# Kernel optimization log

Measured on AMD Instinct MI355X. Metric: run time of the kernel, lower is better.

Reference implementation:

```python
import jax, jax.numpy as jnp
import numpy as np

D_MODEL = 768
D_STATE = 16
D_CONV = 4
EXPAND = 2
D_INNER = EXPAND * D_MODEL  # 1536
DT_RANK = -(-D_MODEL // 16)  # ceil(768/16) = 48
BATCH = 1
SEQ = 2048


def _silu(v):
    return v * jax.nn.sigmoid(v)


def setup_inputs() -> dict:
    key = jax.random.key(0)
    ks = jax.random.split(key, 8)
    s = 0.02
    x = jax.random.normal(ks[0], (BATCH, SEQ, D_MODEL), jnp.float32)
    in_proj_w = jax.random.normal(ks[1], (2 * D_INNER, D_MODEL), jnp.float32) * s
    conv_w = jax.random.normal(ks[2], (D_INNER, 1, D_CONV), jnp.float32) * s  # depthwise, groups=D_INNER
    conv_b = jnp.zeros((D_INNER,), jnp.float32)
    x_proj_w = jax.random.normal(ks[3], (DT_RANK + 2 * D_STATE, D_INNER), jnp.float32) * s
    dt_proj_w = jax.random.normal(ks[4], (D_INNER, DT_RANK), jnp.float32) * s
    dt_proj_b = jax.random.normal(ks[5], (D_INNER,), jnp.float32) * 0.01
    # A = repeat_interleave(arange(1, d_state+1), d_inner rows); A_log = log(A)
    A_log = jnp.log(jnp.tile(jnp.arange(1, D_STATE + 1, dtype=jnp.float32)[None, :], (D_INNER, 1)))
    D = jnp.ones((D_INNER,), jnp.float32)
    out_proj_w = jax.random.normal(ks[6], (D_MODEL, D_INNER), jnp.float32) * s
    return {"x": x, "in_proj_w": in_proj_w, "conv_w": conv_w, "conv_b": conv_b,
            "x_proj_w": x_proj_w, "dt_proj_w": dt_proj_w, "dt_proj_b": dt_proj_b,
            "A_log": A_log, "D": D, "out_proj_w": out_proj_w}


def reference(x, in_proj_w, conv_w, conv_b, x_proj_w, dt_proj_w, dt_proj_b, A_log, D, out_proj_w):
    b, L, d = x.shape
    # in_proj then split into x-branch and gate z
    xz = x @ in_proj_w.T                       # (b, L, 2*d_inner)
    xh, z = jnp.split(xz, 2, axis=-1)          # each (b, L, d_inner)
    # causal depthwise conv1d: torch pads d_conv-1 both sides then slices [:L];
    # equivalent to left-pad d_conv-1, right-pad 0
    xc = jnp.transpose(xh, (0, 2, 1))          # (b, d_inner, L)
    xc = jax.lax.conv_general_dilated(
        xc, conv_w, window_strides=(1,), padding=[(D_CONV - 1, 0)],
        feature_group_count=D_INNER, dimension_numbers=("NCH", "OIH", "NCH"))
    xc = xc + conv_b[None, :, None]
    u = _silu(jnp.transpose(xc, (0, 2, 1)))    # (b, L, d_inner)
    # input-dependent dt, B, C
    x_dbl = u @ x_proj_w.T                     # (b, L, dt_rank + 2*d_state)
    dt, Bm, Cm = jnp.split(x_dbl, [DT_RANK, DT_RANK + D_STATE], axis=-1)
    dt = jax.nn.softplus(dt @ dt_proj_w.T + dt_proj_b)  # (b, L, d_inner)
    A = -jnp.exp(A_log)                        # (d_inner, d_state)
    # selective scan via cumprod/cumsum (faithful to source math)
    dA = jnp.exp(dt[..., None] * A[None, None])              # (b, L, d_inner, d_state)
    dBu = dt[..., None] * Bm[:, :, None, :] * u[..., None]   # (b, L, d_inner, d_state)
    p = jnp.cumprod(dA, axis=1)
    eps = jnp.finfo(u.dtype).eps
    p_safe = jnp.maximum(p, eps)
    g = jnp.cumsum(dBu / p_safe, axis=1)
    h = g * p
    y = jnp.sum(h * Cm[:, :, None, :], axis=-1) + D * u      # (b, L, d_inner)
    y = y * _silu(z)
    return y @ out_proj_w.T                    # (b, L, d_model); dropout=identity (eval)
```

## Files before the change

kernel.cpp:

```cpp
#include <hip/hip_runtime.h>
#include <hip/hip_bf16.h>

#define LSEQ 2048
#define DMODEL 768
#define DINNER 1536
#define DSTATE 16
#define DTRANK 48
#define XDBL_W (DTRANK + 2*DSTATE)
#define CHUNK 32
#define NCHUNK (LSEQ / CHUNK)
#define NDN (DINNER * DSTATE)
#define FEPS 1.1920928955078125e-07f
#define SPLITK 8
#define OSPLIT 4
#define LDST2 36

typedef short bf16x8 __attribute__((ext_vector_type(8)));
typedef float f32x4 __attribute__((ext_vector_type(4)));
typedef unsigned short u16;

__device__ __forceinline__ u16 f2bf_rn(float f) {
    unsigned u = __float_as_uint(f);
    unsigned r = u + 0x7FFFu + ((u >> 16) & 1u);
    return (u16)(r >> 16);
}
__device__ __forceinline__ float bf2f(u16 h) {
    return __uint_as_float(((unsigned)h) << 16);
}

template<int CTRL>
__device__ __forceinline__ float qperm(float x) {
    return __int_as_float(__builtin_amdgcn_update_dpp(
        0, __float_as_int(x), CTRL, 0xF, 0xF, true));
}

__global__ __launch_bounds__(256) void cvt_split(
    const float* __restrict__ src, u16* __restrict__ hi, u16* __restrict__ lo, int n)
{
    int i = (blockIdx.x * 256 + threadIdx.x) * 4;
    if (i >= n) return;
    float4 v = *(const float4*)&src[i];
    u16 h0 = f2bf_rn(v.x), h1 = f2bf_rn(v.y), h2 = f2bf_rn(v.z), h3 = f2bf_rn(v.w);
    u16 l0 = f2bf_rn(v.x - bf2f(h0));
    u16 l1 = f2bf_rn(v.y - bf2f(h1));
    u16 l2 = f2bf_rn(v.z - bf2f(h2));
    u16 l3 = f2bf_rn(v.w - bf2f(h3));
    *(ushort4*)&hi[i] = make_ushort4(h0, h1, h2, h3);
    *(ushort4*)&lo[i] = make_ushort4(l0, l1, l2, l3);
}

__global__ __launch_bounds__(256) void mfma_gemm_tn(
    const u16* __restrict__ Ahi, const u16* __restrict__ Alo,
    const u16* __restrict__ Bhi, const u16* __restrict__ Blo,
    float* __restrict__ C, int ldc, int ldk, int Klen)
{
    __shared__ u16 lds[2 * 4 * 4096];
    const int tid = threadIdx.x;
    const int wid = tid >> 6;
    const int lane = tid & 63;
    const int m0 = blockIdx.x * 128;
    const int n0 = blockIdx.y * 128;
    const int Koff = blockIdx.z * Klen;

    const int st_subrow = lane >> 2;
    const int st_cphys = lane & 3;
    const u16* myplane = (wid == 0) ? Ahi : (wid == 1) ? Alo : (wid == 2) ? Bhi : Blo;
    const int rowbase = (wid < 2) ? m0 : n0;

    f32x4 acc[4][4] = {};
    const int wm = (wid >> 1) * 64;
    const int wn = (wid & 1) * 64;
    const int fr = lane & 15;
    const int fc = lane >> 4;
    const int nsteps = Klen / 32;

    auto stage = [&](int buf, int k0) {
#pragma unroll
        for (int j = 0; j < 8; ++j) {
            int row = j * 16 + st_subrow;
            int clog = st_cphys ^ ((row >> 1) & 3);
            const u16* g = myplane + (size_t)(rowbase + row) * ldk + k0 + clog * 8;
            u16* l = &lds[buf * 16384 + wid * 4096 + j * 512];
            __builtin_amdgcn_global_load_lds(
                (const __attribute__((address_space(1))) unsigned int*)g,
                (__attribute__((address_space(3))) unsigned int*)l, 16, 0, 0);
        }
    };

    stage(0, Koff);
    int cur = 0;
    for (int t = 0; t < nsteps; ++t) {
        __syncthreads();
        if (t + 1 < nsteps) stage(cur ^ 1, Koff + (t + 1) * 32);

        bf16x8 ah[4], al[4], bh[4], bl[4];
        const bf16x8* L = (const bf16x8*)&lds[cur * 16384];
#pragma unroll
        for (int mi = 0; mi < 4; ++mi) {
            int r = wm + mi * 16 + fr;
            int idx = r * 4 + (fc ^ ((r >> 1) & 3));
            ah[mi] = L[idx];
            al[mi] = L[512 + idx];
        }
#pragma unroll
        for (int nj = 0; nj < 4; ++nj) {
            int r = wn + nj * 16 + fr;
            int idx = r * 4 + (fc ^ ((r >> 1) & 3));
            bh[nj] = L[1024 + idx];
            bl[nj] = L[1536 + idx];
        }
#pragma unroll
        for (int mi = 0; mi < 4; ++mi)
#pragma unroll
            for (int nj = 0; nj < 4; ++nj) {
                acc[mi][nj] = __builtin_amdgcn_mfma_f32_16x16x32_bf16(ah[mi], bh[nj], acc[mi][nj], 0, 0, 0);
                acc[mi][nj] = __builtin_amdgcn_mfma_f32_16x16x32_bf16(ah[mi], bl[nj], acc[mi][nj], 0, 0, 0);
                acc[mi][nj] = __builtin_amdgcn_mfma_f32_16x16x32_bf16(al[mi], bh[nj], acc[mi][nj], 0, 0, 0);
            }
        cur ^= 1;
    }

    float* Cz = C + (size_t)blockIdx.z * LSEQ * ldc;
#pragma unroll
    for (int mi = 0; mi < 4; ++mi) {
        int row_b = m0 + wm + mi * 16 + (lane >> 4) * 4;
#pragma unroll
        for (int nj = 0; nj < 4; ++nj) {
            int col = n0 + wn + nj * 16 + (lane & 15);
#pragma unroll
            for (int r = 0; r < 4; ++r)
                Cz[(size_t)(row_b + r) * ldc + col] = acc[mi][nj][r];
        }
    }
}

__global__ __launch_bounds__(256) void reduce4(
    const float* __restrict__ Ppart, float* __restrict__ out, int n)
{
    int i = (blockIdx.x * 256 + threadIdx.x) * 4;
    if (i >= n) return;
    float4 a0 = *(const float4*)&Ppart[i];
    float4 a1 = *(const float4*)&Ppart[(size_t)n + i];
    float4 a2 = *(const float4*)&Ppart[(size_t)2 * n + i];
    float4 a3 = *(const float4*)&Ppart[(size_t)3 * n + i];
    float4 r;
    r.x = ((a0.x + a1.x) + a2.x) + a3.x;
    r.y = ((a0.y + a1.y) + a2.y) + a3.y;
    r.z = ((a0.z + a1.z) + a2.z) + a3.z;
    r.w = ((a0.w + a1.w) + a2.w) + a3.w;
    *(float4*)&out[i] = r;
}

template<int EPI>
__global__ __launch_bounds__(256) void gemm_tn(
    const float* __restrict__ A, int lda,
    const float* __restrict__ B, int ldb,
    float* __restrict__ C, int ldc,
    int M, int N, int K,
    const float* __restrict__ bias)
{
    __shared__ float As[16][64 + 4];
    __shared__ float Bs[16][64 + 4];
    const int tid = threadIdx.x;
    const int m0 = blockIdx.x * 64;
    const int n0 = blockIdx.y * 64;
    const int tx = tid & 15;
    const int ty = tid >> 4;
    const int lr = tid >> 4;
    const int lc = tid & 15;
    float acc[4][4] = {};

    for (int k0 = 0; k0 < K; k0 += 16) {
        const int k = k0 + lc;
#pragma unroll
        for (int i = 0; i < 4; ++i) {
            int m = m0 + lr + i * 16;
            As[lc][lr + i * 16] = (m < M) ? A[(size_t)m * lda + k] : 0.f;
        }
#pragma unroll
        for (int i = 0; i < 4; ++i) {
            int n = n0 + lr + i * 16;
            Bs[lc][lr + i * 16] = (n < N) ? B[(size_t)n * ldb + k] : 0.f;
        }
        __syncthreads();
#pragma unroll
        for (int kk = 0; kk < 16; ++kk) {
            float a[4], b[4];
#pragma unroll
            for (int i = 0; i < 4; ++i) a[i] = As[kk][ty * 4 + i];
#pragma unroll
            for (int j = 0; j < 4; ++j) b[j] = Bs[kk][tx * 4 + j];
#pragma unroll
            for (int i = 0; i < 4; ++i)
#pragma unroll
                for (int j = 0; j < 4; ++j)
                    acc[i][j] = fmaf(a[i], b[j], acc[i][j]);
        }
        __syncthreads();
    }

#pragma unroll
    for (int i = 0; i < 4; ++i) {
        int m = m0 + ty * 4 + i;
        if (m >= M) continue;
#pragma unroll
        for (int j = 0; j < 4; ++j) {
            int n = n0 + tx * 4 + j;
            if (n >= N) continue;
            float v = acc[i][j];
            if (EPI == 1) {
                v += bias[n];
                v = fmaxf(v, 0.f) + log1pf(expf(-fabsf(v)));
            }
            C[(size_t)m * ldc + n] = v;
        }
    }
}

__global__ __launch_bounds__(256) void gemm_tn_splitk(
    const float* __restrict__ A, int lda,
    const float* __restrict__ B, int ldb,
    float* __restrict__ Cpart, int ldc,
    int M, int N, int Kchunk)
{
    __shared__ float As[16][64 + 4];
    __shared__ float Bs[16][64 + 4];
    const int tid = threadIdx.x;
    const int m0 = blockIdx.x * 64;
    const int n0 = blockIdx.y * 64;
    const int kb = blockIdx.z * Kchunk;
    const int tx = tid & 15;
    const int ty = tid >> 4;
    const int lr = tid >> 4;
    const int lc = tid & 15;
    float acc[4][4] = {};

    for (int k0 = kb; k0 < kb + Kchunk; k0 += 16) {
        const int k = k0 + lc;
#pragma unroll
        for (int i = 0; i < 4; ++i) {
            int m = m0 + lr + i * 16;
            As[lc][lr + i * 16] = (m < M) ? A[(size_t)m * lda + k] : 0.f;
        }
#pragma unroll
        for (int i = 0; i < 4; ++i) {
            int n = n0 + lr + i * 16;
            Bs[lc][lr + i * 16] = (n < N) ? B[(size_t)n * ldb + k] : 0.f;
        }
        __syncthreads();
#pragma unroll
        for (int kk = 0; kk < 16; ++kk) {
            float a[4], b[4];
#pragma unroll
            for (int i = 0; i < 4; ++i) a[i] = As[kk][ty * 4 + i];
#pragma unroll
            for (int j = 0; j < 4; ++j) b[j] = Bs[kk][tx * 4 + j];
#pragma unroll
            for (int i = 0; i < 4; ++i)
#pragma unroll
                for (int j = 0; j < 4; ++j)
                    acc[i][j] = fmaf(a[i], b[j], acc[i][j]);
        }
        __syncthreads();
    }

    float* Cs = Cpart + (size_t)blockIdx.z * M * ldc;
#pragma unroll
    for (int i = 0; i < 4; ++i) {
        int m = m0 + ty * 4 + i;
        if (m >= M) continue;
#pragma unroll
        for (int j = 0; j < 4; ++j) {
            int n = n0 + tx * 4 + j;
            if (n >= N) continue;
            Cs[(size_t)m * ldc + n] = acc[i][j];
        }
    }
}

__global__ __launch_bounds__(256) void splitk_reduce(
    const float* __restrict__ Ppart, float* __restrict__ out, int n)
{
    int i = blockIdx.x * 256 + threadIdx.x;
    if (i >= n) return;
    float s = 0.f;
#pragma unroll
    for (int z = 0; z < SPLITK; ++z) s += Ppart[(size_t)z * n + i];
    out[i] = s;
}

__global__ __launch_bounds__(256) void conv_silu_kernel(
    const float* __restrict__ xz,
    const float* __restrict__ conv_w,
    const float* __restrict__ conv_b,
    float* __restrict__ u)
{
    int idx = blockIdx.x * blockDim.x + threadIdx.x;
    if (idx >= LSEQ * DINNER) return;
    int d = idx % DINNER;
    int t = idx / DINNER;
    float w[4];
#pragma unroll
    for (int j = 0; j < 4; ++j) w[j] = conv_w[d * 4 + j];
    float acc = conv_b[d];
#pragma unroll
    for (int j = 0; j < 4; ++j) {
        int s = t - 3 + j;
        if (s >= 0) acc = fmaf(xz[(size_t)s * (2 * DINNER) + d], w[j], acc);
    }
    float sig = 1.f / (1.f + __expf(-acc));
    u[idx] = acc * sig;
}

__global__ __launch_bounds__(256) void scan_chunkprod(
    const float* __restrict__ dtm,
    const float* __restrict__ A_log,
    float* __restrict__ P)
{
    __shared__ float sdtT[16][LDST2];
    const int tid = threadIdx.x;
    const int d0 = blockIdx.x * 16;
    const int t0 = blockIdx.y * CHUNK;
    const int r = tid >> 4, c = tid & 15;
#pragma unroll
    for (int i = 0; i < 2; ++i) {
        int t = r + i * 16;
        sdtT[c][t] = dtm[(size_t)(t0 + t) * DINNER + d0 + c];
    }
    __syncthreads();
    const int n = tid & 15, dl = tid >> 4;
    const float Acoef = -expf(A_log[(d0 + dl) * DSTATE + n]);
    float s = 0.f;
#pragma unroll
    for (int tb = 0; tb < CHUNK / 4; ++tb) {
        f32x4 q = *(const f32x4*)&sdtT[dl][tb * 4];
        s += q[0] + q[1] + q[2] + q[3];
    }
    P[(size_t)blockIdx.y * NDN + d0 * DSTATE + tid] = __expf(Acoef * s);
}

template<int PROD>
__global__ __launch_bounds__(256) void scan_exclusive(float* __restrict__ buf)
{
    const int dn = blockIdx.x * 256 + threadIdx.x;
    float v[NCHUNK];
#pragma unroll
    for (int c = 0; c < NCHUNK; ++c)
        v[c] = buf[(size_t)c * NDN + dn];
    float run = PROD ? 1.f : 0.f;
#pragma unroll
    for (int c = 0; c < NCHUNK; ++c) {
        float t = v[c];
        v[c] = run;
        run = PROD ? run * t : run + t;
    }
#pragma unroll
    for (int c = 0; c < NCHUNK; ++c)
        buf[(size_t)c * NDN + dn] = v[c];
}

__global__ __launch_bounds__(256) void scan_chunksum(
    const float* __restrict__ dtm,
    const float* __restrict__ u,
    const float* __restrict__ xdbl,
    const float* __restrict__ A_log,
    const float* __restrict__ Ppre,
    float* __restrict__ S)
{
    __shared__ float sdtT[16][LDST2], sduT[16][LDST2], sBT[16][LDST2];
    const int tid = threadIdx.x;
    const int d0 = blockIdx.x * 16;
    const int t0 = blockIdx.y * CHUNK;
    const int r = tid >> 4, c = tid & 15;
#pragma unroll
    for (int i = 0; i < 2; ++i) {
        int t = r + i * 16;
        size_t row = (size_t)(t0 + t);
        float dtv = dtm[row * DINNER + d0 + c];
        sdtT[c][t] = dtv;
        sduT[c][t] = dtv * u[row * DINNER + d0 + c];
        sBT[c][t]  = xdbl[row * XDBL_W + DTRANK + c];
    }
    __syncthreads();
    const int n = tid & 15, dl = tid >> 4;
    const float Acoef = -expf(A_log[(d0 + dl) * DSTATE + n]);
    const float Pp = Ppre[(size_t)blockIdx.y * NDN + d0 * DSTATE + tid];
    float s = 0.f, acc = 0.f;
#pragma unroll
    for (int tb = 0; tb < CHUNK / 4; ++tb) {
        f32x4 dq  = *(const f32x4*)&sdtT[dl][tb * 4];
        f32x4 duq = *(const f32x4*)&sduT[dl][tb * 4];
        f32x4 bq  = *(const f32x4*)&sBT[n][tb * 4];
#pragma unroll
        for (int j = 0; j < 4; ++j) {
            s += dq[j];
            float p = Pp * __expf(Acoef * s);
            acc += __fdividef(duq[j] * bq[j], fmaxf(p, FEPS));
        }
    }
    S[(size_t)blockIdx.y * NDN + d0 * DSTATE + tid] = acc;
}

__global__ __launch_bounds__(256) void scan_final(
    const float* __restrict__ dtm,
    const float* __restrict__ u,
    const float* __restrict__ xdbl,
    const float* __restrict__ A_log,
    const float* __restrict__ Ppre,
    const float* __restrict__ Gpre,
    float* __restrict__ xz)
{
    __shared__ float sdtT[64][LDST2], sduT[64][LDST2];
    __shared__ float sBT[16][LDST2], sCT[16][LDST2];
    const int tid = threadIdx.x;
    const int d0 = blockIdx.x * 64;
    const int t0 = blockIdx.y * CHUNK;

#pragma unroll
    for (int i = 0; i < 8; ++i) {
        int idx = i * 256 + tid;
        int dl = idx & 63, tl = idx >> 6;
        size_t row = (size_t)(t0 + tl);
        float dtv = dtm[row * DINNER + d0 + dl];
        sdtT[dl][tl] = dtv;
        sduT[dl][tl] = dtv * u[row * DINNER + d0 + dl];
    }
#pragma unroll
    for (int i = 0; i < 2; ++i) {
        int idx = i * 256 + tid;
        int n = idx & 15, tl = idx >> 4;
        size_t row = (size_t)(t0 + tl);
        sBT[n][tl] = xdbl[row * XDBL_W + DTRANK + n];
        sCT[n][tl] = xdbl[row * XDBL_W + DTRANK + DSTATE + n];
    }
    __syncthreads();

    const int lane = tid & 63, wid = tid >> 6;
    const int dloc = wid * 16 + (lane >> 2);
    const int d = d0 + dloc;
    const int nq = lane & 3;

    f32x4 Ar = *(const f32x4*)&A_log[d * DSTATE + nq * 4];
    float Ac[4] = {-expf(Ar[0]), -expf(Ar[1]), -expf(Ar[2]), -expf(Ar[3])};
    size_t pgbase = (size_t)blockIdx.y * NDN + (size_t)d * DSTATE + nq * 4;
    f32x4 Pp = *(const f32x4*)&Ppre[pgbase];
    f32x4 g = *(const f32x4*)&Gpre[pgbase];
    float s = 0.f;

#pragma unroll
    for (int tb = 0; tb < CHUNK / 4; ++tb) {
        f32x4 dq  = *(const f32x4*)&sdtT[dloc][tb * 4];
        f32x4 duq = *(const f32x4*)&sduT[dloc][tb * 4];
        f32x4 b0 = *(const f32x4*)&sBT[nq * 4 + 0][tb * 4];
        f32x4 b1 = *(const f32x4*)&sBT[nq * 4 + 1][tb * 4];
        f32x4 b2 = *(const f32x4*)&sBT[nq * 4 + 2][tb * 4];
        f32x4 b3 = *(const f32x4*)&sBT[nq * 4 + 3][tb * 4];
        f32x4 c0 = *(const f32x4*)&sCT[nq * 4 + 0][tb * 4];
        f32x4 c1 = *(const f32x4*)&sCT[nq * 4 + 1][tb * 4];
        f32x4 c2 = *(const f32x4*)&sCT[nq * 4 + 2][tb * 4];
        f32x4 c3 = *(const f32x4*)&sCT[nq * 4 + 3][tb * 4];
#pragma unroll
        for (int j = 0; j < 4; ++j) {
            float duv = duq[j];
            s += dq[j];
            float p0 = Pp[0] * __expf(Ac[0] * s);
            float p1 = Pp[1] * __expf(Ac[1] * s);
            float p2 = Pp[2] * __expf(Ac[2] * s);
            float p3 = Pp[3] * __expf(Ac[3] * s);
            g[0] += __fdividef(duv * b0[j], fmaxf(p0, FEPS));
            g[1] += __fdividef(duv * b1[j], fmaxf(p1, FEPS));
            g[2] += __fdividef(duv * b2[j], fmaxf(p2, FEPS));
            g[3] += __fdividef(duv * b3[j], fmaxf(p3, FEPS));
            float part = (g[0] * p0) * c0[j];
            part = fmaf(g[1] * p1, c1[j], part);
            part = fmaf(g[2] * p2, c2[j], part);
            part = fmaf(g[3] * p3, c3[j], part);
            part += qperm<0xB1>(part);
            part += qperm<0x4E>(part);
            if (nq == 0)
                xz[(size_t)(t0 + tb * 4 + j) * (2 * DINNER) + d] = part;
        }
    }
}

__global__ __launch_bounds__(256) void gate_kernel(
    const float* __restrict__ xz,
    const float* __restrict__ u,
    const float* __restrict__ Dvec,
    u16* __restrict__ yhi, u16* __restrict__ ylo)
{
    int i4 = (blockIdx.x * 256 + threadIdx.x) * 4;
    if (i4 >= LSEQ * DINNER) return;
    int t = i4 / DINNER;
    int d = i4 - t * DINNER;
    size_t base = (size_t)t * (2 * DINNER) + d;
    float4 part = *(const float4*)&xz[base];
    float4 zv   = *(const float4*)&xz[base + DINNER];
    float4 uv   = *(const float4*)&u[i4];
    float4 Dd   = *(const float4*)&Dvec[d];
    float pa[4] = {part.x, part.y, part.z, part.w};
    float za[4] = {zv.x, zv.y, zv.z, zv.w};
    float ua[4] = {uv.x, uv.y, uv.z, uv.w};
    float Da[4] = {Dd.x, Dd.y, Dd.z, Dd.w};
    u16 ha[4], la[4];
#pragma unroll
    for (int j = 0; j < 4; ++j) {
        float sig = 1.f / (1.f + __expf(-za[j]));
        float yv = (pa[j] + Da[j] * ua[j]) * (za[j] * sig);
        ha[j] = f2bf_rn(yv);
        la[j] = f2bf_rn(yv - bf2f(ha[j]));
    }
    *(ushort4*)&yhi[i4] = make_ushort4(ha[0], ha[1], ha[2], ha[3]);
    *(ushort4*)&ylo[i4] = make_ushort4(la[0], la[1], la[2], la[3]);
}

extern "C" void kernel_launch(void* const* d_in, const int* in_sizes, int n_in,
                              void* d_out, int out_size, void* d_ws, size_t ws_size,
                              hipStream_t stream) {
    const float* x          = (const float*)d_in[0];
    const float* in_proj_w  = (const float*)d_in[1];
    const float* conv_w     = (const float*)d_in[2];
    const float* conv_b     = (const float*)d_in[3];
    const float* x_proj_w   = (const float*)d_in[4];
    const float* dt_proj_w  = (const float*)d_in[5];
    const float* dt_proj_b  = (const float*)d_in[6];
    const float* A_log      = (const float*)d_in[7];
    const float* Dvec       = (const float*)d_in[8];
    const float* out_proj_w = (const float*)d_in[9];
    float* out = (float*)d_out;

    char* w = (char*)d_ws;
    auto alloc = [&](size_t bytes) { char* p = w; w += (bytes + 255) & ~(size_t)255; return p; };

    float* xz    = (float*)alloc((size_t)LSEQ * 2 * DINNER * 4);
    float* u     = (float*)alloc((size_t)LSEQ * DINNER * 4);
    float* xdbl  = (float*)alloc((size_t)LSEQ * XDBL_W * 4);
    float* dtb   = (float*)alloc((size_t)LSEQ * DINNER * 4);
    float* P     = (float*)alloc((size_t)NCHUNK * NDN * 4);
    float* S     = (float*)alloc((size_t)NCHUNK * NDN * 4);
    float* Ppart = (float*)alloc((size_t)SPLITK * LSEQ * XDBL_W * 4);
    u16* xhi  = (u16*)alloc((size_t)LSEQ * DMODEL * 2);
    u16* xlo  = (u16*)alloc((size_t)LSEQ * DMODEL * 2);
    u16* wihi = (u16*)alloc((size_t)2 * DINNER * DMODEL * 2);
    u16* wilo = (u16*)alloc((size_t)2 * DINNER * DMODEL * 2);
    u16* owhi = (u16*)alloc((size_t)DMODEL * DINNER * 2);
    u16* owlo = (u16*)alloc((size_t)DMODEL * DINNER * 2);
    u16* yhi  = (u16*)alloc((size_t)LSEQ * DINNER * 2);
    u16* ylo  = (u16*)alloc((size_t)LSEQ * DINNER * 2);
    float* opart = u;

    dim3 blk(256);

    cvt_split<<<(LSEQ * DMODEL) / 1024, blk, 0, stream>>>(x, xhi, xlo, LSEQ * DMODEL);
    cvt_split<<<(2 * DINNER * DMODEL) / 1024, blk, 0, stream>>>(in_proj_w, wihi, wilo, 2 * DINNER * DMODEL);
    cvt_split<<<(DMODEL * DINNER) / 1024, blk, 0, stream>>>(out_proj_w, owhi, owlo, DMODEL * DINNER);

    mfma_gemm_tn<<<dim3(LSEQ / 128, (2 * DINNER) / 128, 1), blk, 0, stream>>>(
        xhi, xlo, wihi, wilo, xz, 2 * DINNER, DMODEL, DMODEL);

    conv_silu_kernel<<<(LSEQ * DINNER + 255) / 256, blk, 0, stream>>>(xz, conv_w, conv_b, u);

    gemm_tn_splitk<<<dim3(LSEQ / 64, (XDBL_W + 63) / 64, SPLITK), blk, 0, stream>>>(
        u, DINNER, x_proj_w, DINNER, Ppart, XDBL_W, LSEQ, XDBL_W, DINNER / SPLITK);
    splitk_reduce<<<(LSEQ * XDBL_W + 255) / 256, blk, 0, stream>>>(Ppart, xdbl, LSEQ * XDBL_W);

    gemm_tn<1><<<dim3(LSEQ / 64, DINNER / 64), blk, 0, stream>>>(
        xdbl, XDBL_W, dt_proj_w, DTRANK, dtb, DINNER, LSEQ, DINNER, DTRANK, dt_proj_b);

    scan_chunkprod<<<dim3(DINNER / 16, NCHUNK), blk, 0, stream>>>(dtb, A_log, P);
    scan_exclusive<1><<<NDN / 256, blk, 0, stream>>>(P);
    scan_chunksum<<<dim3(DINNER / 16, NCHUNK), blk, 0, stream>>>(dtb, u, xdbl, A_log, P, S);
    scan_exclusive<0><<<NDN / 256, blk, 0, stream>>>(S);
    scan_final<<<dim3(DINNER / 64, NCHUNK), blk, 0, stream>>>(
        dtb, u, xdbl, A_log, P, S, xz);

    gate_kernel<<<(LSEQ * DINNER) / 1024, blk, 0, stream>>>(xz, u, Dvec, yhi, ylo);

    mfma_gemm_tn<<<dim3(LSEQ / 128, DMODEL / 128, OSPLIT), blk, 0, stream>>>(
        yhi, ylo, owhi, owlo, opart, DMODEL, DINNER, DINNER / OSPLIT);
    reduce4<<<(LSEQ * DMODEL) / 1024, blk, 0, stream>>>(opart, out, LSEQ * DMODEL);
}
```

Baseline: 235.3 us.

## Merge conversion kernels, shrink MFMA GEMM N-tile, vectorize conv over time

Three weight/input bf16 split conversions are merged into one launch, removing two kernel launches. The MFMA GEMM tile changes from 128x128 to 128x64, which doubles the block count for the in/out projections to improve CU occupancy on a 256-CU part, at the cost of less operand reuse per block. The conv+SiLU kernel now computes four consecutive time steps per thread and shares the loaded inputs across them, cutting redundant global loads.

```diff
diff --git a/kernel.cpp b/kernel.cpp
--- a/kernel.cpp
+++ b/kernel.cpp
@@ -34,19 +34,24 @@
         0, __float_as_int(x), CTRL, 0xF, 0xF, true));
 }
 
-__global__ __launch_bounds__(256) void cvt_split(
-    const float* __restrict__ src, u16* __restrict__ hi, u16* __restrict__ lo, int n)
-{
-    int i = (blockIdx.x * 256 + threadIdx.x) * 4;
-    if (i >= n) return;
-    float4 v = *(const float4*)&src[i];
+__global__ __launch_bounds__(256) void cvt_all(
+    const float* __restrict__ w_in,  u16* __restrict__ wihi, u16* __restrict__ wilo, int n1,
+    const float* __restrict__ w_out, u16* __restrict__ owhi, u16* __restrict__ owlo, int n2,
+    const float* __restrict__ x,     u16* __restrict__ xhi,  u16* __restrict__ xlo)
+{
+    int i4 = (blockIdx.x * 256 + threadIdx.x) * 4;
+    const float* src; u16* hi; u16* lo; int off;
+    if (i4 < n1)            { src = w_in;  hi = wihi; lo = wilo; off = i4; }
+    else if (i4 < n1 + n2)  { src = w_out; hi = owhi; lo = owlo; off = i4 - n1; }
+    else                    { src = x;     hi = xhi;  lo = xlo;  off = i4 - n1 - n2; }
+    float4 v = *(const float4*)&src[off];
     u16 h0 = f2bf_rn(v.x), h1 = f2bf_rn(v.y), h2 = f2bf_rn(v.z), h3 = f2bf_rn(v.w);
     u16 l0 = f2bf_rn(v.x - bf2f(h0));
     u16 l1 = f2bf_rn(v.y - bf2f(h1));
     u16 l2 = f2bf_rn(v.z - bf2f(h2));
     u16 l3 = f2bf_rn(v.w - bf2f(h3));
-    *(ushort4*)&hi[i] = make_ushort4(h0, h1, h2, h3);
-    *(ushort4*)&lo[i] = make_ushort4(l0, l1, l2, l3);
+    *(ushort4*)&hi[off] = make_ushort4(h0, h1, h2, h3);
+    *(ushort4*)&lo[off] = make_ushort4(l0, l1, l2, l3);
 }
 
 __global__ __launch_bounds__(256) void mfma_gemm_tn(
@@ -54,22 +59,24 @@
     const u16* __restrict__ Bhi, const u16* __restrict__ Blo,
     float* __restrict__ C, int ldc, int ldk, int Klen)
 {
-    __shared__ u16 lds[2 * 4 * 4096];
+    __shared__ u16 lds[2 * 12288];
     const int tid = threadIdx.x;
     const int wid = tid >> 6;
     const int lane = tid & 63;
     const int m0 = blockIdx.x * 128;
-    const int n0 = blockIdx.y * 128;
+    const int n0 = blockIdx.y * 64;
     const int Koff = blockIdx.z * Klen;
 
     const int st_subrow = lane >> 2;
     const int st_cphys = lane & 3;
     const u16* myplane = (wid == 0) ? Ahi : (wid == 1) ? Alo : (wid == 2) ? Bhi : Blo;
     const int rowbase = (wid < 2) ? m0 : n0;
-
-    f32x4 acc[4][4] = {};
+    const int nIss = (wid < 2) ? 8 : 4;
+    const int planeOff = (wid < 2) ? wid * 4096 : 8192 + (wid - 2) * 2048;
+
+    f32x4 acc[4][2] = {};
     const int wm = (wid >> 1) * 64;
-    const int wn = (wid & 1) * 64;
+    const int wn = (wid & 1) * 32;
     const int fr = lane & 15;
     const int fc = lane >> 4;
     const int nsteps = Klen / 32;
@@ -77,13 +84,15 @@
     auto stage = [&](int buf, int k0) {
 #pragma unroll
         for (int j = 0; j < 8; ++j) {
-            int row = j * 16 + st_subrow;
-            int clog = st_cphys ^ ((row >> 1) & 3);
-            const u16* g = myplane + (size_t)(rowbase + row) * ldk + k0 + clog * 8;
-            u16* l = &lds[buf * 16384 + wid * 4096 + j * 512];
-            __builtin_amdgcn_global_load_lds(
-                (const __attribute__((address_space(1))) unsigned int*)g,
-                (__attribute__((address_space(3))) unsigned int*)l, 16, 0, 0);
+            if (j < nIss) {
+                int row = j * 16 + st_subrow;
+                int clog = st_cphys ^ ((row >> 1) & 3);
+                const u16* g = myplane + (size_t)(rowbase + row) * ldk + k0 + clog * 8;
+                u16* l = &lds[buf * 12288 + planeOff + j * 512];
+                __builtin_amdgcn_global_load_lds(
+                    (const __attribute__((address_space(1))) unsigned int*)g,
+                    (__attribute__((address_space(3))) unsigned int*)l, 16, 0, 0);
+            }
         }
     };
 
@@ -93,8 +102,8 @@
         __syncthreads();
         if (t + 1 < nsteps) stage(cur ^ 1, Koff + (t + 1) * 32);
 
-        bf16x8 ah[4], al[4], bh[4], bl[4];
-        const bf16x8* L = (const bf16x8*)&lds[cur * 16384];
+        bf16x8 ah[4], al[4], bh[2], bl[2];
+        const bf16x8* L = (const bf16x8*)&lds[cur * 12288];
 #pragma unroll
         for (int mi = 0; mi < 4; ++mi) {
             int r = wm + mi * 16 + fr;
@@ -103,16 +112,16 @@
             al[mi] = L[512 + idx];
         }
 #pragma unroll
-        for (int nj = 0; nj < 4; ++nj) {
+        for (int nj = 0; nj < 2; ++nj) {
             int r = wn + nj * 16 + fr;
             int idx = r * 4 + (fc ^ ((r >> 1) & 3));
             bh[nj] = L[1024 + idx];
-            bl[nj] = L[1536 + idx];
+            bl[nj] = L[1280 + idx];
         }
 #pragma unroll
         for (int mi = 0; mi < 4; ++mi)
 #pragma unroll
-            for (int nj = 0; nj < 4; ++nj) {
+            for (int nj = 0; nj < 2; ++nj) {
                 acc[mi][nj] = __builtin_amdgcn_mfma_f32_16x16x32_bf16(ah[mi], bh[nj], acc[mi][nj], 0, 0, 0);
                 acc[mi][nj] = __builtin_amdgcn_mfma_f32_16x16x32_bf16(ah[mi], bl[nj], acc[mi][nj], 0, 0, 0);
                 acc[mi][nj] = __builtin_amdgcn_mfma_f32_16x16x32_bf16(al[mi], bh[nj], acc[mi][nj], 0, 0, 0);
@@ -125,7 +134,7 @@
     for (int mi = 0; mi < 4; ++mi) {
         int row_b = m0 + wm + mi * 16 + (lane >> 4) * 4;
 #pragma unroll
-        for (int nj = 0; nj < 4; ++nj) {
+        for (int nj = 0; nj < 2; ++nj) {
             int col = n0 + wn + nj * 16 + (lane & 15);
 #pragma unroll
             for (int r = 0; r < 4; ++r)
@@ -295,21 +304,28 @@
     const float* __restrict__ conv_b,
     float* __restrict__ u)
 {
-    int idx = blockIdx.x * blockDim.x + threadIdx.x;
-    if (idx >= LSEQ * DINNER) return;
+    int idx = blockIdx.x * 256 + threadIdx.x;
     int d = idx % DINNER;
-    int t = idx / DINNER;
+    int t0 = (idx / DINNER) * 4;
     float w[4];
 #pragma unroll
     for (int j = 0; j < 4; ++j) w[j] = conv_w[d * 4 + j];
-    float acc = conv_b[d];
-#pragma unroll
-    for (int j = 0; j < 4; ++j) {
-        int s = t - 3 + j;
-        if (s >= 0) acc = fmaf(xz[(size_t)s * (2 * DINNER) + d], w[j], acc);
-    }
-    float sig = 1.f / (1.f + __expf(-acc));
-    u[idx] = acc * sig;
+    const float b = conv_b[d];
+    float xv[7];
+#pragma unroll
+    for (int k = 0; k < 7; ++k) {
+        int s = t0 - 3 + k;
+        xv[k] = (s >= 0) ? xz[(size_t)s * (2 * DINNER) + d] : 0.f;
+    }
+#pragma unroll
+    for (int i = 0; i < 4; ++i) {
+        float acc = b;
+#pragma unroll
+        for (int j = 0; j < 4; ++j)
+            acc = fmaf(xv[i + j], w[j], acc);
+        float sig = 1.f / (1.f + __expf(-acc));
+        u[(size_t)(t0 + i) * DINNER + d] = acc * sig;
+    }
 }
 
 __global__ __launch_bounds__(256) void scan_chunkprod(
@@ -551,14 +567,18 @@
 
     dim3 blk(256);
 
-    cvt_split<<<(LSEQ * DMODEL) / 1024, blk, 0, stream>>>(x, xhi, xlo, LSEQ * DMODEL);
-    cvt_split<<<(2 * DINNER * DMODEL) / 1024, blk, 0, stream>>>(in_proj_w, wihi, wilo, 2 * DINNER * DMODEL);
-    cvt_split<<<(DMODEL * DINNER) / 1024, blk, 0, stream>>>(out_proj_w, owhi, owlo, DMODEL * DINNER);
-
-    mfma_gemm_tn<<<dim3(LSEQ / 128, (2 * DINNER) / 128, 1), blk, 0, stream>>>(
+    {
+        int n1 = 2 * DINNER * DMODEL;
+        int n2 = DMODEL * DINNER;
+        int n3 = LSEQ * DMODEL;
+        cvt_all<<<(n1 + n2 + n3) / 1024, blk, 0, stream>>>(
+            in_proj_w, wihi, wilo, n1, out_proj_w, owhi, owlo, n2, x, xhi, xlo);
+    }
+
+    mfma_gemm_tn<<<dim3(LSEQ / 128, (2 * DINNER) / 64, 1), blk, 0, stream>>>(
         xhi, xlo, wihi, wilo, xz, 2 * DINNER, DMODEL, DMODEL);
 
-    conv_silu_kernel<<<(LSEQ * DINNER + 255) / 256, blk, 0, stream>>>(xz, conv_w, conv_b, u);
+    conv_silu_kernel<<<(LSEQ / 4) * DINNER / 256, blk, 0, stream>>>(xz, conv_w, conv_b, u);
 
     gemm_tn_splitk<<<dim3(LSEQ / 64, (XDBL_W + 63) / 64, SPLITK), blk, 0, stream>>>(
         u, DINNER, x_proj_w, DINNER, Ppart, XDBL_W, LSEQ, XDBL_W, DINNER / SPLITK);
@@ -576,7 +596,7 @@
 
     gate_kernel<<<(LSEQ * DINNER) / 1024, blk, 0, stream>>>(xz, u, Dvec, yhi, ylo);
 
-    mfma_gemm_tn<<<dim3(LSEQ / 128, DMODEL / 128, OSPLIT), blk, 0, stream>>>(
+    mfma_gemm_tn<<<dim3(LSEQ / 128, DMODEL / 64, OSPLIT), blk, 0, stream>>>(
         yhi, ylo, owhi, owlo, opart, DMODEL, DINNER, DINNER / OSPLIT);
     reduce4<<<(LSEQ * DMODEL) / 1024, blk, 0, stream>>>(opart, out, LSEQ * DMODEL);
 }
```

Measured after the change: 223.5 us. 1.05x faster.
